# Performance work log

Measured on AMD Instinct MI355X. Metric: run time of the kernel, lower is better.

The kernel has to match this reference:

```python
import jax, jax.numpy as jnp
import numpy as np

D_MODEL, D_K, D_FF, N = 1024, 128, 4096, 8192

def _linear_params(key, fan_in, fan_out):
    # mimic torch nn.Linear default init (uniform +/- 1/sqrt(fan_in))
    k1, k2 = jax.random.split(key)
    bound = 1.0 / np.sqrt(fan_in)
    W = jax.random.uniform(k1, (fan_out, fan_in), jnp.float32, -bound, bound)
    b = jax.random.uniform(k2, (fan_out,), jnp.float32, -bound, bound)
    return W, b

def setup_inputs() -> dict:
    key = jax.random.key(0)
    ks = jax.random.split(key, 7)
    x = jax.random.normal(ks[0], (N, D_MODEL), jnp.float32)
    Wq, bq = _linear_params(ks[1], D_MODEL, D_K)
    Wk, bk = _linear_params(ks[2], D_MODEL, D_K)
    Wv, bv = _linear_params(ks[3], D_MODEL, D_K)
    Wp, bp = _linear_params(ks[4], D_K, D_MODEL)
    W1, b1 = _linear_params(ks[5], D_MODEL, D_FF)
    W2, b2 = _linear_params(ks[6], D_FF, D_MODEL)
    return {"x": x, "Wq": Wq, "bq": bq, "Wk": Wk, "bk": bk, "Wv": Wv, "bv": bv,
            "Wp": Wp, "bp": bp, "W1": W1, "b1": b1, "W2": W2, "b2": b2}

def reference(x, Wq, bq, Wk, bk, Wv, bv, Wp, bp, W1, b1, W2, b2):
    # projections (torch Linear: x @ W.T + b)
    Q = x @ Wq.T + bq            # [n, d_k]
    K = x @ Wk.T + bk            # [n, d_k]
    V = x @ Wv.T + bv            # [n, d_k]
    # linear attention, original evaluation order: (Q @ K^T) @ V
    attn = Q @ K.T               # [n, n]
    context = attn @ V           # [n, d_k]
    out = context @ Wp.T + bp    # [n, d_model]
    x = x + out                  # residual 1
    h = jax.nn.relu(x @ W1.T + b1)  # [n, d_ff]
    return x + (h @ W2.T + b2)   # residual 2
```

## Files before the change

kernel.cpp:

```cpp
#include <hip/hip_runtime.h>


#define MROWS 8192
#define DMODEL 1024
#define DK 128
#define DFF 4096

typedef __attribute__((ext_vector_type(8))) __bf16 bf16x8;
typedef __attribute__((ext_vector_type(4))) float f32x4;

#define BAR()     __builtin_amdgcn_s_barrier()
#define WAITV(n)  asm volatile("s_waitcnt vmcnt(" #n ")" ::: "memory")
#define LGKMC(n)  asm volatile("s_waitcnt lgkmcnt(" #n ")" ::: "memory")
#define SCHED0()  __builtin_amdgcn_sched_barrier(0)
#define GLOAD(src, dst) __builtin_amdgcn_global_load_lds( \
    (const __attribute__((address_space(1))) void*)(src), \
    (__attribute__((address_space(3))) void*)(dst), 16, 0, 0)

#define LDSO(p) ((unsigned)(unsigned long long) \
    (__attribute__((address_space(3))) const char*)(const char*)(p))

__device__ __forceinline__ bf16x8 ldsr(unsigned off) {
    bf16x8 r;
    asm volatile("ds_read_b128 %0, %1" : "=v"(r) : "v"(off));
    return r;
}

__global__ __launch_bounds__(256) void cast_f32_bf16(
    const float* __restrict__ src, __bf16* __restrict__ dst, int n8)
{
    for (int i = blockIdx.x * blockDim.x + threadIdx.x; i < n8;
         i += gridDim.x * blockDim.x) {
        const float4 a = reinterpret_cast<const float4*>(src)[2 * i];
        const float4 b = reinterpret_cast<const float4*>(src)[2 * i + 1];
        bf16x8 o;
        o[0] = (__bf16)a.x; o[1] = (__bf16)a.y; o[2] = (__bf16)a.z; o[3] = (__bf16)a.w;
        o[4] = (__bf16)b.x; o[5] = (__bf16)b.y; o[6] = (__bf16)b.z; o[7] = (__bf16)b.w;
        reinterpret_cast<bf16x8*>(dst)[i] = o;
    }
}

__device__ __forceinline__ void cast_one(const float* s, __bf16* d, int i) {
    const float4 a = reinterpret_cast<const float4*>(s)[2 * i];
    const float4 b = reinterpret_cast<const float4*>(s)[2 * i + 1];
    bf16x8 o;
    o[0] = (__bf16)a.x; o[1] = (__bf16)a.y; o[2] = (__bf16)a.z; o[3] = (__bf16)a.w;
    o[4] = (__bf16)b.x; o[5] = (__bf16)b.y; o[6] = (__bf16)b.z; o[7] = (__bf16)b.w;
    reinterpret_cast<bf16x8*>(d)[i] = o;
}

__global__ __launch_bounds__(256) void cast6(
    const float* __restrict__ s0, __bf16* __restrict__ d0,
    const float* __restrict__ s1, __bf16* __restrict__ d1,
    const float* __restrict__ s2, __bf16* __restrict__ d2,
    const float* __restrict__ s3, __bf16* __restrict__ d3,
    const float* __restrict__ s4, __bf16* __restrict__ d4,
    const float* __restrict__ s5, __bf16* __restrict__ d5)
{
    const int b = blockIdx.x, t = threadIdx.x;
    if      (b <  64)  cast_one(s0, d0, b * 256 + t);
    else if (b < 128)  cast_one(s1, d1, (b - 64) * 256 + t);
    else if (b < 192)  cast_one(s2, d2, (b - 128) * 256 + t);
    else if (b < 256)  cast_one(s3, d3, (b - 192) * 256 + t);
    else if (b < 2304) cast_one(s4, d4, (b - 256) * 256 + t);
    else               cast_one(s5, d5, (b - 2304) * 256 + t);
}

__global__ void pack_bias3(const float* __restrict__ a, const float* __restrict__ b,
                           const float* __restrict__ c, float* __restrict__ o)
{
    const int t = threadIdx.x;
    o[t] = a[t]; o[128 + t] = b[t]; o[256 + t] = c[t];
}

__global__ __launch_bounds__(256) void ffn2_reduce(
    float* __restrict__ y, const __bf16* __restrict__ P0,
    const __bf16* __restrict__ P1, const float* __restrict__ b2, int n8)
{
    for (int i = blockIdx.x * blockDim.x + threadIdx.x; i < n8;
         i += gridDim.x * blockDim.x) {
        const int col0 = (i << 3) & (DMODEL - 1);
        const float4 ba = *reinterpret_cast<const float4*>(&b2[col0]);
        const float4 bb = *reinterpret_cast<const float4*>(&b2[col0 + 4]);
        float4 o0 = reinterpret_cast<const float4*>(y)[2 * i];
        float4 o1 = reinterpret_cast<const float4*>(y)[2 * i + 1];
        const bf16x8 p0 = reinterpret_cast<const bf16x8*>(P0)[i];
        const bf16x8 p1 = reinterpret_cast<const bf16x8*>(P1)[i];
        o0.x += (float)p0[0] + (float)p1[0] + ba.x;
        o0.y += (float)p0[1] + (float)p1[1] + ba.y;
        o0.z += (float)p0[2] + (float)p1[2] + ba.z;
        o0.w += (float)p0[3] + (float)p1[3] + ba.w;
        o1.x += (float)p0[4] + (float)p1[4] + bb.x;
        o1.y += (float)p0[5] + (float)p1[5] + bb.y;
        o1.z += (float)p0[6] + (float)p1[6] + bb.z;
        o1.w += (float)p0[7] + (float)p1[7] + bb.w;
        reinterpret_cast<float4*>(y)[2 * i]     = o0;
        reinterpret_cast<float4*>(y)[2 * i + 1] = o1;
    }
}

template<bool RELU, bool RESID, bool BIAS, bool OUTBF, bool DUAL>
__global__ __launch_bounds__(256) void gemm128(
    const __bf16* __restrict__ A, int lda,
    const __bf16* __restrict__ W,
    const float* __restrict__ bias,
    const float* __restrict__ resid,
    void* __restrict__ Cout, __bf16* __restrict__ Cbf, int ldc, int K)
{
    constexpr int BK = 32;
    __shared__ __bf16 As[128 * BK];
    __shared__ __bf16 Bs[128 * BK];

    const int tid  = threadIdx.x;
    const int lane = tid & 63;
    const int w    = tid >> 6;
    const int wm   = w >> 1;
    const int wn   = w & 1;
    const int fr   = lane & 15;
    const int fq   = lane >> 4;

    const long row0 = (long)blockIdx.y * 128;
    const long col0 = (long)blockIdx.x * 128;

    const int sr = (w << 4) + (lane >> 2);
    const int sc = (lane & 3) << 3;

    const __bf16* gA0 = A + (row0 + sr) * (long)lda + sc;
    const __bf16* gA1 = A + (row0 + 64 + sr) * (long)lda + sc;
    const __bf16* gW0 = W + (col0 + sr) * (long)K + sc;
    const __bf16* gW1 = W + (col0 + 64 + sr) * (long)K + sc;

    __bf16* lA0 = &As[(w << 4) * BK];
    __bf16* lA1 = &As[((w << 4) + 64) * BK];
    __bf16* lB0 = &Bs[(w << 4) * BK];
    __bf16* lB1 = &Bs[((w << 4) + 64) * BK];

    f32x4 acc[4][4] = {};

    for (int k0 = 0; k0 < K; k0 += BK) {
        GLOAD(gA0 + k0, lA0);
        GLOAD(gA1 + k0, lA1);
        GLOAD(gW0 + k0, lB0);
        GLOAD(gW1 + k0, lB1);
        __syncthreads();

        bf16x8 af[4], bfr[4];
        #pragma unroll
        for (int m = 0; m < 4; m++)
            af[m] = *reinterpret_cast<const bf16x8*>(
                &As[(wm * 64 + m * 16 + fr) * BK + fq * 8]);
        #pragma unroll
        for (int n = 0; n < 4; n++)
            bfr[n] = *reinterpret_cast<const bf16x8*>(
                &Bs[(wn * 64 + n * 16 + fr) * BK + fq * 8]);

        #pragma unroll
        for (int m = 0; m < 4; m++)
            #pragma unroll
            for (int n = 0; n < 4; n++)
                acc[m][n] = __builtin_amdgcn_mfma_f32_16x16x32_bf16(
                    af[m], bfr[n], acc[m][n], 0, 0, 0);
        __syncthreads();
    }

    float bc[4];
    #pragma unroll
    for (int n = 0; n < 4; n++)
        bc[n] = BIAS ? bias[col0 + wn * 64 + n * 16 + fr] : 0.0f;
    #pragma unroll
    for (int m = 0; m < 4; m++) {
        #pragma unroll
        for (int j = 0; j < 4; j++) {
            const long r = row0 + wm * 64 + m * 16 + fq * 4 + j;
            #pragma unroll
            for (int n = 0; n < 4; n++) {
                const long c = col0 + wn * 64 + n * 16 + fr;
                float v = acc[m][n][j] + bc[n];
                if constexpr (RESID) v += resid[r * ldc + c];
                if constexpr (RELU)  v = fmaxf(v, 0.0f);
                if constexpr (OUTBF) ((__bf16*)Cout)[r * ldc + c] = (__bf16)v;
                else                 ((float*)Cout)[r * ldc + c] = v;
                if constexpr (DUAL)  Cbf[r * ldc + c] = (__bf16)v;
            }
        }
    }
}

#define RD_B()                                             \
    _Pragma("unroll")                                      \
    for (int n = 0; n < 4; n++) {                          \
        bb[n][0] = ldsr(pB + rb0 + n * 2048);              \
        bb[n][1] = ldsr(pB + rb1 + n * 2048);              \
    }
#define RD_A(m0_, cnt_)                                    \
    _Pragma("unroll")                                      \
    for (int m = m0_; m < m0_ + cnt_; m++) {               \
        a[m][0] = ldsr(pA + rb0 + m * 2048);               \
        a[m][1] = ldsr(pA + rb1 + m * 2048);               \
    }
#define MFMA2(m0_)                                                            \
    _Pragma("unroll")                                                         \
    for (int m = m0_; m < m0_ + 2; m++)                                       \
        _Pragma("unroll")                                                     \
        for (int n = 0; n < 4; n++) {                                         \
            acc[m][n] = __builtin_amdgcn_mfma_f32_16x16x32_bf16(              \
                a[m][0], bb[n][0], acc[m][n], 0, 0, 0);                       \
            acc[m][n] = __builtin_amdgcn_mfma_f32_16x16x32_bf16(              \
                a[m][1], bb[n][1], acc[m][n], 0, 0, 0);                       \
        }

template<bool RELU, bool BIAS>
__global__ __launch_bounds__(256, 2) void gemm256x128(
    const __bf16* __restrict__ A, int lda,
    const __bf16* __restrict__ W, int ldw,
    const float* __restrict__ bias,
    __bf16* __restrict__ Cout, long sstride, int ldc,
    int klen, int nb, int nbx)
{
    __shared__ char lds[49152];

    const int bid = blockIdx.x;
    const int sid = bid / nb;
    const int ib  = bid % nb;
    const int chunk = nb >> 3;
    const int swz   = (ib & 7) * chunk + (ib >> 3);
    const int bx    = swz % nbx;
    const int by    = swz / nbx;

    const long row0 = (long)by * 256;
    const long col0 = (long)bx * 128;

    const __bf16* Ash = A + (long)sid * klen;
    const __bf16* Wsh = W + (long)sid * klen;

    const int tid  = threadIdx.x;
    const int lane = tid & 63;
    const int w    = tid >> 6;
    const int wm   = w >> 1;
    const int wn   = w & 1;
    const int fr   = lane & 15;
    const int fq   = lane >> 4;

    const int scole = ((lane & 7) ^ (lane >> 3)) << 3;
    const __bf16* gA = Ash + (row0 + w * 8 + (lane >> 3)) * (long)lda + scole;
    const __bf16* gB = Wsh + (col0 + w * 8 + (lane >> 3)) * (long)ldw + scole;

    char* ldsc = &lds[0];
    const unsigned lbase = LDSO(ldsc);
    const int nt = klen >> 6;

    auto stage = [&](int t) {
        const __bf16* ap = gA + (long)t * 64;
        const __bf16* bp = gB + (long)t * 64;
        #pragma unroll
        for (int r = 0; r < 8; r++)
            GLOAD(ap + (long)(32 * r) * lda, ldsc + r * 4096 + (w << 10));
        #pragma unroll
        for (int r = 0; r < 4; r++)
            GLOAD(bp + (long)(32 * r) * ldw, ldsc + 32768 + r * 4096 + (w << 10));
    };

    const unsigned rb0 = fr * 128 + ((fq * 16) ^ ((fr & 7) << 4));
    const unsigned rb1 = fr * 128 + ((64 + fq * 16) ^ ((fr & 7) << 4));
    const unsigned pA = lbase + (wm << 14);
    const unsigned pB = lbase + 32768 + (wn << 13);

    f32x4 acc[8][4] = {};
    bf16x8 a[8][2], bb[4][2];

    for (int t = 0; t < nt; ++t) {
        stage(t);
        WAITV(0);
        BAR();

        RD_B();
        RD_A(0, 8);

        LGKMC(12); SCHED0();
        __builtin_amdgcn_s_setprio(1); MFMA2(0); __builtin_amdgcn_s_setprio(0);
        LGKMC(8); SCHED0();
        __builtin_amdgcn_s_setprio(1); MFMA2(2); __builtin_amdgcn_s_setprio(0);
        LGKMC(4); SCHED0();
        __builtin_amdgcn_s_setprio(1); MFMA2(4); __builtin_amdgcn_s_setprio(0);
        LGKMC(0); SCHED0();
        __builtin_amdgcn_s_setprio(1); MFMA2(6); __builtin_amdgcn_s_setprio(0);

        BAR();
    }

    __bf16* Cb = Cout + (long)sid * sstride;
    float bc[4];
    #pragma unroll
    for (int n = 0; n < 4; n++)
        bc[n] = BIAS ? bias[col0 + wn * 64 + n * 16 + fr] : 0.0f;

    __bf16* sw = reinterpret_cast<__bf16*>(ldsc) + (w << 12);
    const long crow0 = row0 + wm * 128;
    const long ccol0 = col0 + wn * 64;
    #pragma unroll
    for (int half = 0; half < 2; half++) {
        #pragma unroll
        for (int m = 0; m < 4; m++)
            #pragma unroll
            for (int j = 0; j < 4; j++) {
                const int row = m * 16 + fq * 4 + j;
                #pragma unroll
                for (int n = 0; n < 4; n++) {
                    float v = acc[half * 4 + m][n][j] + bc[n];
                    if constexpr (RELU) v = fmaxf(v, 0.0f);
                    sw[row * 64 + n * 16 + fr] = (__bf16)v;
                }
            }
        #pragma unroll
        for (int i = 0; i < 8; i++) {
            const bf16x8 vv = *reinterpret_cast<const bf16x8*>(sw + i * 512 + lane * 8);
            const int r  = half * 64 + i * 8 + (lane >> 3);
            const int cg = (lane & 7) << 3;
            *reinterpret_cast<bf16x8*>(&Cb[(crow0 + r) * (long)ldc + ccol0 + cg]) = vv;
        }
        __builtin_amdgcn_s_waitcnt(0);
    }
}

__global__ __launch_bounds__(256) void ktv_partial(
    const __bf16* __restrict__ Kp, const __bf16* __restrict__ Vp,
    int ld, float* __restrict__ part)
{
    __shared__ float ks[32][DK];
    __shared__ float vs[32][DK];
    const int tid = threadIdx.x;
    const int ti  = tid >> 4;
    const int tj  = tid & 15;
    float acc[8][8] = {};
    const long base = (long)blockIdx.x * 128;

    for (int n0 = 0; n0 < 128; n0 += 32) {
        for (int t = tid; t < 512; t += 256) {
            const int r  = t >> 4;
            const int cc = (t & 15) << 3;
            const bf16x8 k8 = *reinterpret_cast<const bf16x8*>(
                &Kp[(base + n0 + r) * (long)ld + cc]);
            const bf16x8 v8 = *reinterpret_cast<const bf16x8*>(
                &Vp[(base + n0 + r) * (long)ld + cc]);
            #pragma unroll
            for (int u = 0; u < 8; u++) {
                ks[r][cc + u] = (float)k8[u];
                vs[r][cc + u] = (float)v8[u];
            }
        }
        __syncthreads();
        for (int n = 0; n < 32; n++) {
            float kk[8], vv[8];
            #pragma unroll
            for (int i = 0; i < 8; i++) kk[i] = ks[n][(ti << 3) + i];
            #pragma unroll
            for (int j = 0; j < 8; j++) vv[j] = vs[n][(tj << 3) + j];
            #pragma unroll
            for (int i = 0; i < 8; i++)
                #pragma unroll
                for (int j = 0; j < 8; j++)
                    acc[i][j] = fmaf(kk[i], vv[j], acc[i][j]);
        }
        __syncthreads();
    }

    float* dst = &part[(long)blockIdx.x * (DK * DK)];
    #pragma unroll
    for (int i = 0; i < 8; i++) {
        const int ig = (ti << 3) + i;
        *reinterpret_cast<float4*>(&dst[ig * DK + (tj << 3)]) =
            make_float4(acc[i][0], acc[i][1], acc[i][2], acc[i][3]);
        *reinterpret_cast<float4*>(&dst[ig * DK + (tj << 3) + 4]) =
            make_float4(acc[i][4], acc[i][5], acc[i][6], acc[i][7]);
    }
}

__global__ __launch_bounds__(256) void ktv_reduce(
    const float* __restrict__ part, __bf16* __restrict__ ktvR)
{
    const int t = blockIdx.x * 256 + threadIdx.x;
    float s = 0.0f;
    for (int b = 0; b < 64; b++) s += part[(long)b * (DK * DK) + t];
    ktvR[t] = (__bf16)s;
}

extern "C" void kernel_launch(void* const* d_in, const int* in_sizes, int n_in,
                              void* d_out, int out_size, void* d_ws, size_t ws_size,
                              hipStream_t stream) {
    const float* x  = (const float*)d_in[0];
    const float* Wq = (const float*)d_in[1];
    const float* bq = (const float*)d_in[2];
    const float* Wk = (const float*)d_in[3];
    const float* bk = (const float*)d_in[4];
    const float* Wv = (const float*)d_in[5];
    const float* bv = (const float*)d_in[6];
    const float* Wp = (const float*)d_in[7];
    const float* bp = (const float*)d_in[8];
    const float* W1 = (const float*)d_in[9];
    const float* b1 = (const float*)d_in[10];
    const float* W2 = (const float*)d_in[11];
    const float* b2 = (const float*)d_in[12];
    float* out = (float*)d_out;

    char* ws = (char*)d_ws;
    const size_t MB = 1ull << 20;
    __bf16* xb    = (__bf16*)(ws);
    __bf16* P0b   = (__bf16*)(ws);
    __bf16* P1b   = P0b + (long)MROWS * DMODEL;
    __bf16* x2b   = (__bf16*)(ws +  34 * MB);
    __bf16* Hb    = (__bf16*)(ws +  51 * MB);
    __bf16* QKVb  = (__bf16*)(ws + 119 * MB);
    __bf16* W1b   = (__bf16*)(ws + 126 * MB);
    __bf16* W2b   = (__bf16*)(ws + 135 * MB);
    __bf16* Wqkvb = (__bf16*)(ws + 144 * MB);
    __bf16* Wpb   = (__bf16*)(ws + 145 * MB);
    float*  Part  = (float*) (ws + 146 * MB);
    __bf16* KtvRb = (__bf16*)(ws + 151 * MB);
    __bf16* MtB   = (__bf16*)(ws + 152 * MB);
    float*  bqkvf = (float*) (ws + 155 * MB);

    const dim3 blk(256);

    cast_f32_bf16<<<2048, blk, 0, stream>>>(x, xb, MROWS * DMODEL / 8);
    cast6<<<4352, blk, 0, stream>>>(
        Wq, Wqkvb, Wk, Wqkvb + DK * DMODEL, Wv, Wqkvb + 2 * DK * DMODEL,
        Wp, Wpb, W1, W1b, W2, W2b);
    pack_bias3<<<1, 128, 0, stream>>>(bq, bk, bv, bqkvf);

    gemm128<false,false,true,true,false><<<dim3(3, 64), blk, 0, stream>>>(
        xb, DMODEL, Wqkvb, bqkvf, nullptr, QKVb, nullptr, 3 * DK, DMODEL);

    ktv_partial<<<64, blk, 0, stream>>>(QKVb + DK, QKVb + 2 * DK, 3 * DK, Part);
    ktv_reduce <<<64, blk, 0, stream>>>(Part, KtvRb);

    gemm128<false,false,false,true,false><<<dim3(1, 8), blk, 0, stream>>>(
        Wpb, DK, KtvRb, nullptr, nullptr, MtB, nullptr, DK, DK);

    gemm128<false,true,true,false,true><<<dim3(8, 64), blk, 0, stream>>>(
        QKVb, 3 * DK, MtB, bp, x, out, x2b, DMODEL, DK);

    gemm256x128<true,true><<<1024, blk, 0, stream>>>(
        x2b, DMODEL, W1b, DMODEL, b1, Hb, 0, DFF, DMODEL, 1024, DFF / 128);

    gemm256x128<false,false><<<512, blk, 0, stream>>>(
        Hb, DFF, W2b, DFF, nullptr, P0b,
        (long)MROWS * DMODEL, DMODEL, DFF / 2, 256, DMODEL / 128);

    ffn2_reduce<<<2048, blk, 0, stream>>>(out, P0b, P1b, b2, MROWS * DMODEL / 8);
}
```

Measured before the change: 227.6 us.

## Fuse x fp32-to-bf16 cast into QKV GEMM and drop fp32 residual write

```diff
diff --git a/kernel.cpp b/kernel.cpp
--- a/kernel.cpp
+++ b/kernel.cpp
@@ -26,20 +26,6 @@
     return r;
 }
 
-__global__ __launch_bounds__(256) void cast_f32_bf16(
-    const float* __restrict__ src, __bf16* __restrict__ dst, int n8)
-{
-    for (int i = blockIdx.x * blockDim.x + threadIdx.x; i < n8;
-         i += gridDim.x * blockDim.x) {
-        const float4 a = reinterpret_cast<const float4*>(src)[2 * i];
-        const float4 b = reinterpret_cast<const float4*>(src)[2 * i + 1];
-        bf16x8 o;
-        o[0] = (__bf16)a.x; o[1] = (__bf16)a.y; o[2] = (__bf16)a.z; o[3] = (__bf16)a.w;
-        o[4] = (__bf16)b.x; o[5] = (__bf16)b.y; o[6] = (__bf16)b.z; o[7] = (__bf16)b.w;
-        reinterpret_cast<bf16x8*>(dst)[i] = o;
-    }
-}
-
 __device__ __forceinline__ void cast_one(const float* s, __bf16* d, int i) {
     const float4 a = reinterpret_cast<const float4*>(s)[2 * i];
     const float4 b = reinterpret_cast<const float4*>(s)[2 * i + 1];
@@ -73,35 +59,36 @@
     o[t] = a[t]; o[128 + t] = b[t]; o[256 + t] = c[t];
 }
 
-__global__ __launch_bounds__(256) void ffn2_reduce(
-    float* __restrict__ y, const __bf16* __restrict__ P0,
-    const __bf16* __restrict__ P1, const float* __restrict__ b2, int n8)
+__global__ __launch_bounds__(256) void ffn2_reduce2(
+    float* __restrict__ y, const __bf16* __restrict__ x2b,
+    const __bf16* __restrict__ P0, const __bf16* __restrict__ P1,
+    const float* __restrict__ b2, int n8)
 {
     for (int i = blockIdx.x * blockDim.x + threadIdx.x; i < n8;
          i += gridDim.x * blockDim.x) {
         const int col0 = (i << 3) & (DMODEL - 1);
         const float4 ba = *reinterpret_cast<const float4*>(&b2[col0]);
         const float4 bb = *reinterpret_cast<const float4*>(&b2[col0 + 4]);
-        float4 o0 = reinterpret_cast<const float4*>(y)[2 * i];
-        float4 o1 = reinterpret_cast<const float4*>(y)[2 * i + 1];
+        const bf16x8 xx = reinterpret_cast<const bf16x8*>(x2b)[i];
         const bf16x8 p0 = reinterpret_cast<const bf16x8*>(P0)[i];
         const bf16x8 p1 = reinterpret_cast<const bf16x8*>(P1)[i];
-        o0.x += (float)p0[0] + (float)p1[0] + ba.x;
-        o0.y += (float)p0[1] + (float)p1[1] + ba.y;
-        o0.z += (float)p0[2] + (float)p1[2] + ba.z;
-        o0.w += (float)p0[3] + (float)p1[3] + ba.w;
-        o1.x += (float)p0[4] + (float)p1[4] + bb.x;
-        o1.y += (float)p0[5] + (float)p1[5] + bb.y;
-        o1.z += (float)p0[6] + (float)p1[6] + bb.z;
-        o1.w += (float)p0[7] + (float)p1[7] + bb.w;
+        float4 o0, o1;
+        o0.x = (float)xx[0] + (float)p0[0] + (float)p1[0] + ba.x;
+        o0.y = (float)xx[1] + (float)p0[1] + (float)p1[1] + ba.y;
+        o0.z = (float)xx[2] + (float)p0[2] + (float)p1[2] + ba.z;
+        o0.w = (float)xx[3] + (float)p0[3] + (float)p1[3] + ba.w;
+        o1.x = (float)xx[4] + (float)p0[4] + (float)p1[4] + bb.x;
+        o1.y = (float)xx[5] + (float)p0[5] + (float)p1[5] + bb.y;
+        o1.z = (float)xx[6] + (float)p0[6] + (float)p1[6] + bb.z;
+        o1.w = (float)xx[7] + (float)p0[7] + (float)p1[7] + bb.w;
         reinterpret_cast<float4*>(y)[2 * i]     = o0;
         reinterpret_cast<float4*>(y)[2 * i + 1] = o1;
     }
 }
 
-template<bool RELU, bool RESID, bool BIAS, bool OUTBF, bool DUAL>
+template<bool RELU, bool RESID, bool BIAS, bool OUTBF, bool DUAL, bool F32A>
 __global__ __launch_bounds__(256) void gemm128(
-    const __bf16* __restrict__ A, int lda,
+    const void* __restrict__ Ap, int lda,
     const __bf16* __restrict__ W,
     const float* __restrict__ bias,
     const float* __restrict__ resid,
@@ -125,8 +112,11 @@
     const int sr = (w << 4) + (lane >> 2);
     const int sc = (lane & 3) << 3;
 
-    const __bf16* gA0 = A + (row0 + sr) * (long)lda + sc;
-    const __bf16* gA1 = A + (row0 + 64 + sr) * (long)lda + sc;
+    const __bf16* gA0 = F32A ? nullptr : (const __bf16*)Ap + (row0 + sr) * (long)lda + sc;
+    const __bf16* gA1 = F32A ? nullptr : (const __bf16*)Ap + (row0 + 64 + sr) * (long)lda + sc;
+    const float*  gAf = F32A ? (const float*)Ap + (row0 + (tid >> 1)) * (long)lda
+                               + ((tid & 1) << 4)
+                             : nullptr;
     const __bf16* gW0 = W + (col0 + sr) * (long)K + sc;
     const __bf16* gW1 = W + (col0 + 64 + sr) * (long)K + sc;
 
@@ -138,8 +128,24 @@
     f32x4 acc[4][4] = {};
 
     for (int k0 = 0; k0 < K; k0 += BK) {
-        GLOAD(gA0 + k0, lA0);
-        GLOAD(gA1 + k0, lA1);
+        if constexpr (F32A) {
+            const float* s = gAf + k0;
+            const float4 f0 = reinterpret_cast<const float4*>(s)[0];
+            const float4 f1 = reinterpret_cast<const float4*>(s)[1];
+            const float4 f2 = reinterpret_cast<const float4*>(s)[2];
+            const float4 f3 = reinterpret_cast<const float4*>(s)[3];
+            bf16x8 o0, o1;
+            o0[0] = (__bf16)f0.x; o0[1] = (__bf16)f0.y; o0[2] = (__bf16)f0.z; o0[3] = (__bf16)f0.w;
+            o0[4] = (__bf16)f1.x; o0[5] = (__bf16)f1.y; o0[6] = (__bf16)f1.z; o0[7] = (__bf16)f1.w;
+            o1[0] = (__bf16)f2.x; o1[1] = (__bf16)f2.y; o1[2] = (__bf16)f2.z; o1[3] = (__bf16)f2.w;
+            o1[4] = (__bf16)f3.x; o1[5] = (__bf16)f3.y; o1[6] = (__bf16)f3.z; o1[7] = (__bf16)f3.w;
+            const int ar = tid >> 1, ac = (tid & 1) << 4;
+            *reinterpret_cast<bf16x8*>(&As[ar * BK + ac])     = o0;
+            *reinterpret_cast<bf16x8*>(&As[ar * BK + ac + 8]) = o1;
+        } else {
+            GLOAD(gA0 + k0, lA0);
+            GLOAD(gA1 + k0, lA1);
+        }
         GLOAD(gW0 + k0, lB0);
         GLOAD(gW1 + k0, lB1);
         __syncthreads();
@@ -404,7 +410,6 @@
 
     char* ws = (char*)d_ws;
     const size_t MB = 1ull << 20;
-    __bf16* xb    = (__bf16*)(ws);
     __bf16* P0b   = (__bf16*)(ws);
     __bf16* P1b   = P0b + (long)MROWS * DMODEL;
     __bf16* x2b   = (__bf16*)(ws +  34 * MB);
@@ -421,23 +426,22 @@
 
     const dim3 blk(256);
 
-    cast_f32_bf16<<<2048, blk, 0, stream>>>(x, xb, MROWS * DMODEL / 8);
     cast6<<<4352, blk, 0, stream>>>(
         Wq, Wqkvb, Wk, Wqkvb + DK * DMODEL, Wv, Wqkvb + 2 * DK * DMODEL,
         Wp, Wpb, W1, W1b, W2, W2b);
     pack_bias3<<<1, 128, 0, stream>>>(bq, bk, bv, bqkvf);
 
-    gemm128<false,false,true,true,false><<<dim3(3, 64), blk, 0, stream>>>(
-        xb, DMODEL, Wqkvb, bqkvf, nullptr, QKVb, nullptr, 3 * DK, DMODEL);
+    gemm128<false,false,true,true,false,true><<<dim3(3, 64), blk, 0, stream>>>(
+        x, DMODEL, Wqkvb, bqkvf, nullptr, QKVb, nullptr, 3 * DK, DMODEL);
 
     ktv_partial<<<64, blk, 0, stream>>>(QKVb + DK, QKVb + 2 * DK, 3 * DK, Part);
     ktv_reduce <<<64, blk, 0, stream>>>(Part, KtvRb);
 
-    gemm128<false,false,false,true,false><<<dim3(1, 8), blk, 0, stream>>>(
+    gemm128<false,false,false,true,false,false><<<dim3(1, 8), blk, 0, stream>>>(
         Wpb, DK, KtvRb, nullptr, nullptr, MtB, nullptr, DK, DK);
 
-    gemm128<false,true,true,false,true><<<dim3(8, 64), blk, 0, stream>>>(
-        QKVb, 3 * DK, MtB, bp, x, out, x2b, DMODEL, DK);
+    gemm128<false,true,true,true,false,false><<<dim3(8, 64), blk, 0, stream>>>(
+        QKVb, 3 * DK, MtB, bp, x, x2b, nullptr, DMODEL, DK);
 
     gemm256x128<true,true><<<1024, blk, 0, stream>>>(
         x2b, DMODEL, W1b, DMODEL, b1, Hb, 0, DFF, DMODEL, 1024, DFF / 128);
@@ -446,5 +450,6 @@
         Hb, DFF, W2b, DFF, nullptr, P0b,
         (long)MROWS * DMODEL, DMODEL, DFF / 2, 256, DMODEL / 128);
 
-    ffn2_reduce<<<2048, blk, 0, stream>>>(out, P0b, P1b, b2, MROWS * DMODEL / 8);
-}
+    ffn2_reduce2<<<2048, blk, 0, stream>>>(out, x2b, P0b, P1b, b2,
+                                           MROWS * DMODEL / 8);
+}
```

Result: no change. 223.8 us (-1.7%).
